# Optimization experiments

Hardware: AMD Instinct MI355X
Metric: run time of the kernel (lower is better)

Reference implementation:

```python
import jax, jax.numpy as jnp
import numpy as np

TEMPERATURE = 0.1
WEIGHT = 0.1
EPS = 1e-12  # F.normalize clamp_min eps

B = 512   # number of reactions (batches)
G = 128   # atoms per reaction per side (uniform groups)
D = 256   # feature dim


def setup_inputs() -> dict:
    key = jax.random.key(0)
    k1, k2, k3, k4 = jax.random.split(key, 4)
    preds = jax.random.normal(k1, (B,), dtype=jnp.float32)
    y = jax.random.normal(k2, (B,), dtype=jnp.float32)
    reactant_features = jax.random.normal(k3, (B * G, D), dtype=jnp.float32)
    product_features = jax.random.normal(k4, (B * G, D), dtype=jnp.float32)
    # sorted, uniform-size groups: [0]*G, [1]*G, ...
    batch_idx = jnp.repeat(jnp.arange(B, dtype=jnp.int64), G)
    return {
        "preds": preds,
        "y": y,
        "reactant_features": reactant_features,
        "product_features": product_features,
        "reactant_batch_indices": batch_idx,
        "product_batch_indices": batch_idx,
    }


def _l2_normalize(x):
    # matches F.normalize(p=2, dim=1): x / max(||x||, eps)
    n = jnp.sqrt(jnp.sum(x * x, axis=-1, keepdims=True))
    return x / jnp.maximum(n, EPS)


def reference(preds, y, reactant_features, product_features,
              reactant_batch_indices, product_batch_indices):
    # MSE with reduction='sum'
    mse_loss = jnp.sum((preds - y) ** 2)

    # groups are uniform and sorted -> per-batch gather == reshape
    nb = int(reactant_batch_indices[-1]) + 1          # number of unique batches
    g = reactant_features.shape[0] // nb
    d = reactant_features.shape[1]
    r = reactant_features.reshape(nb, g, d)
    p = product_features.reshape(nb, g, d)

    rn = _l2_normalize(r)
    pn = _l2_normalize(p)
    # per-batch similarity [nb, g, g]
    sim = jnp.einsum('bgd,bhd->bgh', rn, pn) / TEMPERATURE

    # cross_entropy with labels = arange(g), mean over rows (torch default)
    lse = jax.scipy.special.logsumexp(sim, axis=-1)   # [nb, g]
    diag = jnp.einsum('bgg->bg', sim)                 # logits at true labels
    ce_per_batch = jnp.mean(lse - diag, axis=-1)      # [nb]
    contrastive_loss = jnp.mean(ce_per_batch)         # sum over batches / nb

    return mse_loss + WEIGHT * contrastive_loss
```

## Files before the change

### kernel.cpp

```cpp
#include <hip/hip_runtime.h>
#include <hip/hip_bf16.h>
#include <math.h>

#define BATCH 512
#define G 128
#define D 256
#define LRP 264

typedef __attribute__((ext_vector_type(8))) short short8;
typedef __attribute__((ext_vector_type(4))) float f32x4;
typedef __attribute__((ext_vector_type(4))) int  i32x4;

__device__ __forceinline__ unsigned short bfbits(float x) {
    __hip_bfloat16 h = __float2bfloat16(x);
    union { __hip_bfloat16 h; unsigned short u; } c; c.h = h; return c.u;
}
__device__ __forceinline__ unsigned int pack2bf16(float a, float b) {
    return (unsigned int)bfbits(a) | ((unsigned int)bfbits(b) << 16);
}

__global__ __attribute__((amdgpu_flat_work_group_size(512, 512), amdgpu_waves_per_eu(4, 4)))
void fused_kernel(const float* __restrict__ rfeat,
                  const float* __restrict__ pfeat,
                  const float* __restrict__ preds,
                  const float* __restrict__ yv,
                  float* __restrict__ out)
{
    const int b = blockIdx.x;
    const float* rb = rfeat + (size_t)b * (G * D);
    const float* pb = pfeat + (size_t)b * (G * D);

    __shared__ unsigned short ps[64 * LRP];
    __shared__ float inv_r[G];
    __shared__ float inv_p[G];
    __shared__ float red[8];

    const int tid  = threadIdx.x;
    const int lane = tid & 63;
    const int wv   = tid >> 6;
    const int lg   = lane >> 4;
    const int lc   = lane & 15;

    const int srow = tid >> 4;
    const int sc4  = tid & 15;

    float contrib = 0.f;
    if (b == 0) {
        float dd = preds[tid] - yv[tid];
        contrib = dd * dd;
    }

    short8 afr[8];
    float nrsum = 0.f;
    const float* rptr = rb + (wv * 16 + lc) * D + lg * 8;
#pragma unroll
    for (int ks = 0; ks < 8; ++ks) {
        float4 x0 = *reinterpret_cast<const float4*>(rptr + ks * 32);
        float4 x1 = *reinterpret_cast<const float4*>(rptr + ks * 32 + 4);
        nrsum += x0.x*x0.x + x0.y*x0.y + x0.z*x0.z + x0.w*x0.w
               + x1.x*x1.x + x1.y*x1.y + x1.z*x1.z + x1.w*x1.w;
        i32x4 pk = { (int)pack2bf16(x0.x, x0.y), (int)pack2bf16(x0.z, x0.w),
                     (int)pack2bf16(x1.x, x1.y), (int)pack2bf16(x1.z, x1.w) };
        union { i32x4 i; short8 s; } u; u.i = pk;
        afr[ks] = u.s;
    }
    nrsum += __shfl_xor(nrsum, 16);
    nrsum += __shfl_xor(nrsum, 32);
    if (lane < 16)
        inv_r[wv * 16 + lane] = 10.0f / fmaxf(sqrtf(nrsum), 1e-12f);

    float4 pv[2][4];
#pragma unroll
    for (int it = 0; it < 2; ++it)
#pragma unroll
        for (int j = 0; j < 4; ++j)
            pv[it][j] = *reinterpret_cast<const float4*>(pb + (srow + 32 * it) * D + (sc4 + 16 * j) * 4);
#pragma unroll
    for (int it = 0; it < 2; ++it) {
        const int row = srow + 32 * it;
        float s = 0.f;
#pragma unroll
        for (int j = 0; j < 4; ++j) {
            const float4 v = pv[it][j];
            s += v.x*v.x + v.y*v.y + v.z*v.z + v.w*v.w;
            *reinterpret_cast<uint2*>(&ps[row * LRP + (sc4 + 16 * j) * 4]) =
                make_uint2(pack2bf16(v.x, v.y), pack2bf16(v.z, v.w));
        }
#pragma unroll
        for (int off = 1; off < 16; off <<= 1) s += __shfl_xor(s, off);
        if (sc4 == 0) inv_p[row] = 1.0f / fmaxf(sqrtf(s), 1e-12f);
    }
    __syncthreads();

    float4 qv[2][4];
#pragma unroll
    for (int it = 0; it < 2; ++it)
#pragma unroll
        for (int j = 0; j < 4; ++j)
            qv[it][j] = *reinterpret_cast<const float4*>(pb + (64 + srow + 32 * it) * D + (sc4 + 16 * j) * 4);

    f32x4 acc[8];
#pragma unroll
    for (int nj = 0; nj < 8; ++nj) acc[nj] = (f32x4){0.f, 0.f, 0.f, 0.f};

#pragma unroll
    for (int ks = 0; ks < 8; ++ks) {
        const int kb = ks * 32 + lg * 8;
#pragma unroll
        for (int nj = 0; nj < 4; ++nj) {
            short8 bfr = *reinterpret_cast<const short8*>(&ps[(nj * 16 + lc) * LRP + kb]);
            acc[nj] = __builtin_amdgcn_mfma_f32_16x16x32_bf16(afr[ks], bfr, acc[nj], 0, 0, 0);
        }
    }
    __syncthreads();

#pragma unroll
    for (int it = 0; it < 2; ++it) {
        const int row = srow + 32 * it;
        float s = 0.f;
#pragma unroll
        for (int j = 0; j < 4; ++j) {
            const float4 v = qv[it][j];
            s += v.x*v.x + v.y*v.y + v.z*v.z + v.w*v.w;
            *reinterpret_cast<uint2*>(&ps[row * LRP + (sc4 + 16 * j) * 4]) =
                make_uint2(pack2bf16(v.x, v.y), pack2bf16(v.z, v.w));
        }
#pragma unroll
        for (int off = 1; off < 16; off <<= 1) s += __shfl_xor(s, off);
        if (sc4 == 0) inv_p[64 + row] = 1.0f / fmaxf(sqrtf(s), 1e-12f);
    }
    __syncthreads();

#pragma unroll
    for (int ks = 0; ks < 8; ++ks) {
        const int kb = ks * 32 + lg * 8;
#pragma unroll
        for (int nj = 0; nj < 4; ++nj) {
            short8 bfr = *reinterpret_cast<const short8*>(&ps[(nj * 16 + lc) * LRP + kb]);
            acc[4 + nj] = __builtin_amdgcn_mfma_f32_16x16x32_bf16(afr[ks], bfr, acc[4 + nj], 0, 0, 0);
        }
    }

    float invp_r[8];
#pragma unroll
    for (int nj = 0; nj < 8; ++nj) invp_r[nj] = inv_p[nj * 16 + lc];

    const int njd = wv;
    float ce_part = 0.f;
#pragma unroll
    for (int reg = 0; reg < 4; ++reg) {
        const int rrow = lg * 4 + reg;
        const float invr_g = inv_r[wv * 16 + rrow];
        float s[8];
        float m = -3.0e38f;
#pragma unroll
        for (int nj = 0; nj < 8; ++nj) {
            s[nj] = acc[nj][reg] * invr_g * invp_r[nj];
            m = fmaxf(m, s[nj]);
        }
#pragma unroll
        for (int off = 1; off < 16; off <<= 1) m = fmaxf(m, __shfl_xor(m, off));
        float e = 0.f;
#pragma unroll
        for (int nj = 0; nj < 8; ++nj) e += __expf(s[nj] - m);
#pragma unroll
        for (int off = 1; off < 16; off <<= 1) e += __shfl_xor(e, off);
        if (lc == rrow)
            ce_part += (m + __logf(e)) - s[njd];
    }

    contrib += ce_part * (0.1f / ((float)BATCH * (float)G));
#pragma unroll
    for (int off = 1; off < 64; off <<= 1) contrib += __shfl_xor(contrib, off);
    if (lane == 0) red[wv] = contrib;
    __syncthreads();
    if (tid == 0) {
        float t = 0.f;
#pragma unroll
        for (int i = 0; i < 8; ++i) t += red[i];
        atomicAdd(out, t);
    }
}

extern "C" void kernel_launch(void* const* d_in, const int* in_sizes, int n_in,
                              void* d_out, int out_size, void* d_ws, size_t ws_size,
                              hipStream_t stream) {
    const float* preds = (const float*)d_in[0];
    const float* yv    = (const float*)d_in[1];
    const float* rf    = (const float*)d_in[2];
    const float* pf    = (const float*)d_in[3];
    float* out = (float*)d_out;
    (void)d_ws; (void)ws_size;

    hipMemsetAsync(out, 0, (size_t)out_size * sizeof(float), stream);
    fused_kernel<<<BATCH, 512, 0, stream>>>(rf, pf, preds, yv, out);
}
```

Before: 36.29 us.

## Hand-schedule global loads with inline asm and explicit vmcnt waits

Replaces compiler-generated loads with inline-asm global_load_dwordx4 and issues the product and reactant loads in a staged order. Explicit s_waitcnt vmcnt counts and sched barriers let later loads stay in flight while earlier tiles are converted to bf16 and written to LDS. It also drops the waves_per_eu(4,4) hint in favour of plain launch_bounds. Hand-counted waitcnt values are fragile: if the compiler emits any other vector memory operation in between, the counts no longer guard the right loads and the kernel could read data before it arrives.

```diff
diff --git a/kernel.cpp b/kernel.cpp
--- a/kernel.cpp
+++ b/kernel.cpp
@@ -19,7 +19,17 @@
     return (unsigned int)bfbits(a) | ((unsigned int)bfbits(b) << 16);
 }
 
-__global__ __attribute__((amdgpu_flat_work_group_size(512, 512), amdgpu_waves_per_eu(4, 4)))
+__device__ __forceinline__ float4 aload(const float* p) {
+    float4 r;
+    asm volatile("global_load_dwordx4 %0, %1, off" : "=v"(r) : "v"(p));
+    return r;
+}
+
+#define WAITVM(N)  asm volatile("s_waitcnt vmcnt(" #N ")" ::: "memory")
+#define WAITLGKM0  asm volatile("s_waitcnt lgkmcnt(0)" ::: "memory")
+#define SCHED0     __builtin_amdgcn_sched_barrier(0)
+
+__global__ __launch_bounds__(512)
 void fused_kernel(const float* __restrict__ rfeat,
                   const float* __restrict__ pfeat,
                   const float* __restrict__ preds,
@@ -40,7 +50,6 @@
     const int wv   = tid >> 6;
     const int lg   = lane >> 4;
     const int lc   = lane & 15;
-
     const int srow = tid >> 4;
     const int sc4  = tid & 15;
 
@@ -50,13 +59,51 @@
         contrib = dd * dd;
     }
 
+    float4 pv[8];
+#pragma unroll
+    for (int it = 0; it < 2; ++it)
+#pragma unroll
+        for (int j = 0; j < 4; ++j)
+            pv[it * 4 + j] = aload(pb + (srow + 32 * it) * D + (sc4 + 16 * j) * 4);
+
+    const float* rptr = rb + (wv * 16 + lc) * D + lg * 8;
+    float4 rxa[8];
+#pragma unroll
+    for (int ks = 0; ks < 4; ++ks) {
+        rxa[2 * ks]     = aload(rptr + ks * 32);
+        rxa[2 * ks + 1] = aload(rptr + ks * 32 + 4);
+    }
+
+    WAITVM(8); SCHED0;
+#pragma unroll
+    for (int it = 0; it < 2; ++it) {
+        const int row = srow + 32 * it;
+        float s = 0.f;
+#pragma unroll
+        for (int j = 0; j < 4; ++j) {
+            const float4 v = pv[it * 4 + j];
+            s += v.x*v.x + v.y*v.y + v.z*v.z + v.w*v.w;
+            *reinterpret_cast<uint2*>(&ps[row * LRP + (sc4 + 16 * j) * 4]) =
+                make_uint2(pack2bf16(v.x, v.y), pack2bf16(v.z, v.w));
+        }
+#pragma unroll
+        for (int off = 1; off < 16; off <<= 1) s += __shfl_xor(s, off);
+        if (sc4 == 0) inv_p[row] = 1.0f / fmaxf(sqrtf(s), 1e-12f);
+    }
+
+    float4 rxb[8];
+#pragma unroll
+    for (int ks = 0; ks < 4; ++ks) {
+        rxb[2 * ks]     = aload(rptr + (4 + ks) * 32);
+        rxb[2 * ks + 1] = aload(rptr + (4 + ks) * 32 + 4);
+    }
+
+    WAITVM(8); SCHED0;
     short8 afr[8];
     float nrsum = 0.f;
-    const float* rptr = rb + (wv * 16 + lc) * D + lg * 8;
-#pragma unroll
-    for (int ks = 0; ks < 8; ++ks) {
-        float4 x0 = *reinterpret_cast<const float4*>(rptr + ks * 32);
-        float4 x1 = *reinterpret_cast<const float4*>(rptr + ks * 32 + 4);
+#pragma unroll
+    for (int ks = 0; ks < 4; ++ks) {
+        const float4 x0 = rxa[2 * ks], x1 = rxa[2 * ks + 1];
         nrsum += x0.x*x0.x + x0.y*x0.y + x0.z*x0.z + x0.w*x0.w
                + x1.x*x1.x + x1.y*x1.y + x1.z*x1.z + x1.w*x1.w;
         i32x4 pk = { (int)pack2bf16(x0.x, x0.y), (int)pack2bf16(x0.z, x0.w),
@@ -64,72 +111,72 @@
         union { i32x4 i; short8 s; } u; u.i = pk;
         afr[ks] = u.s;
     }
+
+    float4 qv[8];
+#pragma unroll
+    for (int it = 0; it < 2; ++it)
+#pragma unroll
+        for (int j = 0; j < 4; ++j)
+            qv[it * 4 + j] = aload(pb + (64 + srow + 32 * it) * D + (sc4 + 16 * j) * 4);
+
+    WAITVM(8); SCHED0;
+#pragma unroll
+    for (int ks = 0; ks < 4; ++ks) {
+        const float4 x0 = rxb[2 * ks], x1 = rxb[2 * ks + 1];
+        nrsum += x0.x*x0.x + x0.y*x0.y + x0.z*x0.z + x0.w*x0.w
+               + x1.x*x1.x + x1.y*x1.y + x1.z*x1.z + x1.w*x1.w;
+        i32x4 pk = { (int)pack2bf16(x0.x, x0.y), (int)pack2bf16(x0.z, x0.w),
+                     (int)pack2bf16(x1.x, x1.y), (int)pack2bf16(x1.z, x1.w) };
+        union { i32x4 i; short8 s; } u; u.i = pk;
+        afr[4 + ks] = u.s;
+    }
     nrsum += __shfl_xor(nrsum, 16);
     nrsum += __shfl_xor(nrsum, 32);
     if (lane < 16)
         inv_r[wv * 16 + lane] = 10.0f / fmaxf(sqrtf(nrsum), 1e-12f);
 
-    float4 pv[2][4];
-#pragma unroll
-    for (int it = 0; it < 2; ++it)
-#pragma unroll
-        for (int j = 0; j < 4; ++j)
-            pv[it][j] = *reinterpret_cast<const float4*>(pb + (srow + 32 * it) * D + (sc4 + 16 * j) * 4);
+    WAITLGKM0;
+    __builtin_amdgcn_s_barrier();
+    SCHED0;
+
+    f32x4 acc[8];
+#pragma unroll
+    for (int nj = 0; nj < 8; ++nj) acc[nj] = (f32x4){0.f, 0.f, 0.f, 0.f};
+
+#pragma unroll
+    for (int ks = 0; ks < 8; ++ks) {
+        const int kb = ks * 32 + lg * 8;
+#pragma unroll
+        for (int nj = 0; nj < 4; ++nj) {
+            short8 bfr = *reinterpret_cast<const short8*>(&ps[(nj * 16 + lc) * LRP + kb]);
+            acc[nj] = __builtin_amdgcn_mfma_f32_16x16x32_bf16(afr[ks], bfr, acc[nj], 0, 0, 0);
+        }
+    }
+
+    WAITLGKM0;
+    __builtin_amdgcn_s_barrier();
+    SCHED0;
+
+    WAITVM(0); SCHED0;
 #pragma unroll
     for (int it = 0; it < 2; ++it) {
         const int row = srow + 32 * it;
         float s = 0.f;
 #pragma unroll
         for (int j = 0; j < 4; ++j) {
-            const float4 v = pv[it][j];
+            const float4 v = qv[it * 4 + j];
             s += v.x*v.x + v.y*v.y + v.z*v.z + v.w*v.w;
             *reinterpret_cast<uint2*>(&ps[row * LRP + (sc4 + 16 * j) * 4]) =
                 make_uint2(pack2bf16(v.x, v.y), pack2bf16(v.z, v.w));
         }
 #pragma unroll
         for (int off = 1; off < 16; off <<= 1) s += __shfl_xor(s, off);
-        if (sc4 == 0) inv_p[row] = 1.0f / fmaxf(sqrtf(s), 1e-12f);
-    }
-    __syncthreads();
-
-    float4 qv[2][4];
-#pragma unroll
-    for (int it = 0; it < 2; ++it)
-#pragma unroll
-        for (int j = 0; j < 4; ++j)
-            qv[it][j] = *reinterpret_cast<const float4*>(pb + (64 + srow + 32 * it) * D + (sc4 + 16 * j) * 4);
-
-    f32x4 acc[8];
-#pragma unroll
-    for (int nj = 0; nj < 8; ++nj) acc[nj] = (f32x4){0.f, 0.f, 0.f, 0.f};
-
-#pragma unroll
-    for (int ks = 0; ks < 8; ++ks) {
-        const int kb = ks * 32 + lg * 8;
-#pragma unroll
-        for (int nj = 0; nj < 4; ++nj) {
-            short8 bfr = *reinterpret_cast<const short8*>(&ps[(nj * 16 + lc) * LRP + kb]);
-            acc[nj] = __builtin_amdgcn_mfma_f32_16x16x32_bf16(afr[ks], bfr, acc[nj], 0, 0, 0);
-        }
-    }
-    __syncthreads();
-
-#pragma unroll
-    for (int it = 0; it < 2; ++it) {
-        const int row = srow + 32 * it;
-        float s = 0.f;
-#pragma unroll
-        for (int j = 0; j < 4; ++j) {
-            const float4 v = qv[it][j];
-            s += v.x*v.x + v.y*v.y + v.z*v.z + v.w*v.w;
-            *reinterpret_cast<uint2*>(&ps[row * LRP + (sc4 + 16 * j) * 4]) =
-                make_uint2(pack2bf16(v.x, v.y), pack2bf16(v.z, v.w));
-        }
-#pragma unroll
-        for (int off = 1; off < 16; off <<= 1) s += __shfl_xor(s, off);
         if (sc4 == 0) inv_p[64 + row] = 1.0f / fmaxf(sqrtf(s), 1e-12f);
     }
-    __syncthreads();
+
+    WAITLGKM0;
+    __builtin_amdgcn_s_barrier();
+    SCHED0;
 
 #pragma unroll
     for (int ks = 0; ks < 8; ++ks) {
```

After: 40.31 us. +11.1%, slower.
